# Kernel optimization log

Hardware: AMD Instinct MI355X
Metric: run time of the kernel (lower is better)

The kernel has to match this reference:

```python
import jax, jax.numpy as jnp
import numpy as np

DIM = 2048
ATT_DIM = 2048
N_HEADS = 16
HEAD_DIM = ATT_DIM // N_HEADS  # 128


def setup_inputs() -> dict:
    key = jax.random.key(0)
    k1, k2, k3 = jax.random.split(key, 3)
    tgt_len = 2048
    x = jax.random.normal(k1, (tgt_len, DIM), dtype=jnp.float32)
    # nn.Linear weights: [out_features, in_features], no bias
    w_in = jax.random.normal(k2, (3 * ATT_DIM, DIM), dtype=jnp.float32) * (1.0 / np.sqrt(DIM))
    w_out = jax.random.normal(k3, (DIM, ATT_DIM), dtype=jnp.float32) * (1.0 / np.sqrt(ATT_DIM))
    return {"x": x, "w_in": w_in, "w_out": w_out, "tgt_len": tgt_len}


def reference(x, w_in, w_out, tgt_len):
    # qkv projection: Linear -> x @ W^T, then split into thirds
    qkv = x @ w_in.T                      # [T, 3*att_dim]
    q, k, v = jnp.split(qkv, 3, axis=-1)  # each [T, att_dim]
    # [T, H, Dh] -> [H, T, Dh]
    q = q.reshape(tgt_len, N_HEADS, HEAD_DIM).transpose(1, 0, 2)
    k = k.reshape(tgt_len, N_HEADS, HEAD_DIM).transpose(1, 0, 2)
    v = v.reshape(tgt_len, N_HEADS, HEAD_DIM).transpose(1, 0, 2)
    scaling = 1.0 / jnp.sqrt(jnp.asarray(HEAD_DIM, dtype=x.dtype))
    scores = jnp.einsum("htd,hsd->hts", q, k) * scaling  # [H, T, T]
    attn = jax.nn.softmax(scores, axis=-1)
    ctx = jnp.einsum("hts,hsd->htd", attn, v)             # [H, T, Dh]
    ctx = ctx.transpose(1, 0, 2).reshape(tgt_len, ATT_DIM)
    return ctx @ w_out.T                                   # [T, dim]
```

## Files before the change

### kernel.cpp

```cpp
#include <hip/hip_runtime.h>

#define T_LEN 2048
#define DIM 2048
#define NH 16
#define HD 128
#define QKV_LD 6144

typedef __attribute__((ext_vector_type(8))) short short8;
typedef __attribute__((ext_vector_type(4))) float f32x4;
typedef __attribute__((ext_vector_type(4))) float float4v;
typedef __attribute__((ext_vector_type(4))) unsigned short ushort4v;
typedef __attribute__((ext_vector_type(2))) unsigned int uint2v;

static __device__ __forceinline__ unsigned short f2bf(float f) {
  unsigned u = __builtin_bit_cast(unsigned, f);
  u += 0x7fffu + ((u >> 16) & 1u);
  return (unsigned short)(u >> 16);
}

static __device__ __forceinline__ f32x4 mfma16(short8 a, short8 b, f32x4 c) {
  return __builtin_amdgcn_mfma_f32_16x16x32_bf16(a, b, c, 0, 0, 0);
}

#define GLDS16(SRC, DST)                                                            \
  __builtin_amdgcn_global_load_lds((__attribute__((address_space(1))) void*)(SRC),  \
                                   (__attribute__((address_space(3))) void*)(DST),  \
                                   16, 0, 0)

__global__ void cast_f32_bf16(const float* __restrict__ in,
                              unsigned short* __restrict__ out, int n4) {
  int i = blockIdx.x * blockDim.x + threadIdx.x;
  const int stride = gridDim.x * blockDim.x;
  for (; i < n4; i += stride) {
    float4v f = ((const float4v*)in)[i];
    ushort4v o;
    o.x = f2bf(f.x); o.y = f2bf(f.y); o.z = f2bf(f.z); o.w = f2bf(f.w);
    ((ushort4v*)out)[i] = o;
  }
}

template <int OUT_BF16>
__global__ __launch_bounds__(256) void gemm_bt_128(
    const unsigned short* __restrict__ A,
    const unsigned short* __restrict__ B,
    void* __restrict__ Cv, int M, int N, int K) {
  __shared__ unsigned short As[128 * 64];
  __shared__ unsigned short Bs[128 * 64];
  const int tid = threadIdx.x;
  const int wave = tid >> 6;
  const int lane = tid & 63;
  const int l15 = lane & 15, l16 = lane >> 4;
  const int bm = blockIdx.y * 128;
  const int bn = blockIdx.x * 128;
  const int wr = wave >> 1, wc = wave & 1;

  f32x4 acc[4][4] = {};

  int srow[4], scol[4];
#pragma unroll
  for (int i = 0; i < 4; ++i) {
    int lin = i * 4096 + tid * 16;
    int row = lin >> 7;
    int cb = lin & 127;
    srow[i] = row;
    scol[i] = (cb ^ ((row & 7) << 4)) >> 1;
  }

  for (int k0 = 0; k0 < K; k0 += 64) {
#pragma unroll
    for (int i = 0; i < 4; ++i) {
      GLDS16(A + (size_t)(bm + srow[i]) * K + k0 + scol[i], As + i * 2048 + wave * 512);
      GLDS16(B + (size_t)(bn + srow[i]) * K + k0 + scol[i], Bs + i * 2048 + wave * 512);
    }
    __syncthreads();
#pragma unroll
    for (int kk = 0; kk < 2; ++kk) {
      const int cb = kk * 64 + l16 * 16;
      short8 af[4], bfr[4];
#pragma unroll
      for (int m = 0; m < 4; ++m) {
        int row = wr * 64 + m * 16 + l15;
        af[m] = *(const short8*)((const char*)As + row * 128 + (cb ^ ((row & 7) << 4)));
      }
#pragma unroll
      for (int n = 0; n < 4; ++n) {
        int row = wc * 64 + n * 16 + l15;
        bfr[n] = *(const short8*)((const char*)Bs + row * 128 + (cb ^ ((row & 7) << 4)));
      }
#pragma unroll
      for (int m = 0; m < 4; ++m)
#pragma unroll
        for (int n = 0; n < 4; ++n)
          acc[m][n] = mfma16(af[m], bfr[n], acc[m][n]);
    }
    __syncthreads();
  }

#pragma unroll
  for (int m = 0; m < 4; ++m)
#pragma unroll
    for (int n = 0; n < 4; ++n) {
      int row = bm + wr * 64 + m * 16 + l16 * 4;
      int col = bn + wc * 64 + n * 16 + l15;
#pragma unroll
      for (int j = 0; j < 4; ++j) {
        if (OUT_BF16)
          ((unsigned short*)Cv)[(size_t)(row + j) * N + col] = f2bf(acc[m][n][j]);
        else
          ((float*)Cv)[(size_t)(row + j) * N + col] = acc[m][n][j];
      }
    }
}

__global__ __launch_bounds__(256) void transpose_v(
    const unsigned short* __restrict__ qkv, unsigned short* __restrict__ vt) {
  __shared__ unsigned short t[64 * 128];
  const int tid = threadIdx.x;
  const int h = blockIdx.y;
  const int s0 = blockIdx.x * 64;
#pragma unroll
  for (int i = 0; i < 4; ++i) {
    int lin = i * 2048 + tid * 8;
    int row = lin >> 7, col = lin & 127;
    char* dst = (char*)t + row * 256 + ((col * 2) ^ (((row >> 3) & 7) << 4));
    *(short8*)dst =
        *(const short8*)(qkv + (size_t)(s0 + row) * QKV_LD + 2 * DIM + h * HD + col);
  }
  __syncthreads();
#pragma unroll
  for (int i2 = 0; i2 < 4; ++i2) {
    int d = (tid >> 3) + i2 * 32;
    int sb = (tid & 7) * 8;
    short8 v;
#pragma unroll
    for (int j = 0; j < 8; ++j) {
      int s = sb + j;
      v[j] = *(const short*)((const char*)t + s * 256 + ((d * 2) ^ (((s >> 3) & 7) << 4)));
    }
    *(short8*)(vt + ((size_t)h * HD + d) * T_LEN + s0 + sb) = v;
  }
}

__global__ __launch_bounds__(256) void attn_fwd(
    const unsigned short* __restrict__ qkv,
    const unsigned short* __restrict__ vt,
    unsigned short* __restrict__ ctx) {
  __shared__ unsigned short Ks[2][64 * 128];
  __shared__ unsigned short Vs[2][128 * 64];
  __shared__ unsigned short Ps[4 * 16 * 64];
  const int tid = threadIdx.x;
  const int wave = tid >> 6;
  const int lane = tid & 63;
  const int l15 = lane & 15, l16 = lane >> 4;
  const int h = blockIdx.y;
  const int q0 = blockIdx.x * 64 + wave * 16;
  const float SCL = 0.08838834764831845f * 1.4426950408889634f;

  short8 qf[4];
#pragma unroll
  for (int kk = 0; kk < 4; ++kk)
    qf[kk] = *(const short8*)(qkv + (size_t)(q0 + l15) * QKV_LD + h * HD + kk * 32 + l16 * 8);

  f32x4 acc_o[8] = {};
  float m_r = -1e30f;
  float l_r = 0.f;

  int krow[4], kcol[4], vrow[4], vcol[4];
#pragma unroll
  for (int i = 0; i < 4; ++i) {
    int lin = i * 4096 + tid * 16;
    int r = lin >> 8;
    int cb = lin & 255;
    krow[i] = r; kcol[i] = (cb ^ ((r & 7) << 4)) >> 1;
    r = lin >> 7;
    cb = lin & 127;
    vrow[i] = r; vcol[i] = (cb ^ ((r & 7) << 4)) >> 1;
  }
  const unsigned short* kbase = qkv + 2048 + h * HD;
  const unsigned short* vbase = vt + (size_t)h * HD * T_LEN;

#define STAGE_KV(BUF, S0)                                                              \
  do {                                                                                 \
    _Pragma("unroll")                                                                  \
    for (int i = 0; i < 4; ++i) {                                                      \
      GLDS16(kbase + (size_t)((S0) + krow[i]) * QKV_LD + kcol[i],                      \
             Ks[BUF] + i * 2048 + wave * 512);                                         \
      GLDS16(vbase + (size_t)vrow[i] * T_LEN + (S0) + vcol[i],                         \
             Vs[BUF] + i * 2048 + wave * 512);                                         \
    }                                                                                  \
  } while (0)

  STAGE_KV(0, 0);
  __syncthreads();

  const int NT = T_LEN / 64;
  int cur = 0;
  for (int t = 0; t < NT; ++t) {
    if (t + 1 < NT) STAGE_KV(cur ^ 1, (t + 1) * 64);

    const unsigned short* ks = Ks[cur];
    const unsigned short* vs = Vs[cur];

    f32x4 st[4] = {};
#pragma unroll
    for (int c = 0; c < 4; ++c) {
#pragma unroll
      for (int kk = 0; kk < 4; ++kk) {
        int row = c * 16 + l15;
        int cb = kk * 64 + l16 * 16;
        short8 kf = *(const short8*)((const char*)ks + row * 256 + (cb ^ ((row & 7) << 4)));
        st[c] = mfma16(kf, qf[kk], st[c]);
      }
    }

    float pmax = -1e30f;
#pragma unroll
    for (int c = 0; c < 4; ++c)
#pragma unroll
      for (int j = 0; j < 4; ++j)
        pmax = fmaxf(pmax, st[c][j]);
    pmax *= SCL;
    pmax = fmaxf(pmax, __shfl_xor(pmax, 16));
    pmax = fmaxf(pmax, __shfl_xor(pmax, 32));

    if (!__all(pmax - m_r <= 8.0f)) {
      float nm = fmaxf(m_r, pmax);
      float corr = __builtin_amdgcn_exp2f(m_r - nm);
      m_r = nm;
      l_r *= corr;
      float cj[4];
#pragma unroll
      for (int j = 0; j < 4; ++j) cj[j] = __shfl(corr, l16 * 4 + j);
#pragma unroll
      for (int d = 0; d < 8; ++d)
#pragma unroll
        for (int j = 0; j < 4; ++j) acc_o[d][j] *= cj[j];
    }

    float p[4][4];
    float tsum = 0.f;
#pragma unroll
    for (int c = 0; c < 4; ++c)
#pragma unroll
      for (int j = 0; j < 4; ++j) {
        p[c][j] = __builtin_amdgcn_exp2f(st[c][j] * SCL - m_r);
        tsum += p[c][j];
      }
    tsum += __shfl_xor(tsum, 16);
    tsum += __shfl_xor(tsum, 32);
    l_r += tsum;

    char* pbase = (char*)Ps + wave * 2048;
#pragma unroll
    for (int c = 0; c < 4; ++c) {
      uint2v w;
      w.x = (unsigned)f2bf(p[c][0]) | ((unsigned)f2bf(p[c][1]) << 16);
      w.y = (unsigned)f2bf(p[c][2]) | ((unsigned)f2bf(p[c][3]) << 16);
      int off = l15 * 128 + c * 32 + l16 * 8;
      *(uint2v*)(pbase + (off ^ ((l15 & 7) << 4))) = w;
    }

#pragma unroll
    for (int kk = 0; kk < 2; ++kk) {
      int cb = kk * 64 + l16 * 16;
      short8 pa = *(const short8*)(pbase + l15 * 128 + (cb ^ ((l15 & 7) << 4)));
#pragma unroll
      for (int d = 0; d < 8; ++d) {
        int row = d * 16 + l15;
        short8 vb = *(const short8*)((const char*)vs + row * 128 + (cb ^ ((row & 7) << 4)));
        acc_o[d] = mfma16(pa, vb, acc_o[d]);
      }
    }

    __syncthreads();
    cur ^= 1;
  }
#undef STAGE_KV

  float lq[4];
#pragma unroll
  for (int j = 0; j < 4; ++j) lq[j] = 1.0f / __shfl(l_r, l16 * 4 + j);
#pragma unroll
  for (int d = 0; d < 8; ++d)
#pragma unroll
    for (int j = 0; j < 4; ++j) {
      int row = q0 + l16 * 4 + j;
      int col = h * HD + d * 16 + l15;
      ctx[(size_t)row * DIM + col] = f2bf(acc_o[d][j] * lq[j]);
    }
}

extern "C" void kernel_launch(void* const* d_in, const int* in_sizes, int n_in,
                              void* d_out, int out_size, void* d_ws, size_t ws_size,
                              hipStream_t stream) {
  const float* x = (const float*)d_in[0];
  const float* w_in = (const float*)d_in[1];
  const float* w_out = (const float*)d_in[2];

  char* ws = (char*)d_ws;
  unsigned short* xbf  = (unsigned short*)(ws + 0);
  unsigned short* wibf = (unsigned short*)(ws + 8388608);
  unsigned short* wobf = (unsigned short*)(ws + 33554432);
  unsigned short* qkv  = (unsigned short*)(ws + 41943040);
  unsigned short* ctx  = (unsigned short*)(ws + 67108864);
  unsigned short* vt   = (unsigned short*)(ws + 75497472);

  cast_f32_bf16<<<2048, 256, 0, stream>>>(x, xbf, (T_LEN * DIM) / 4);
  cast_f32_bf16<<<2048, 256, 0, stream>>>(w_in, wibf, (3 * DIM * DIM) / 4);
  cast_f32_bf16<<<2048, 256, 0, stream>>>(w_out, wobf, (DIM * DIM) / 4);

  gemm_bt_128<1><<<dim3(48, 16), 256, 0, stream>>>(xbf, wibf, (void*)qkv, T_LEN, 3 * DIM, DIM);
  transpose_v<<<dim3(32, 16), 256, 0, stream>>>(qkv, vt);
  attn_fwd<<<dim3(32, 16), 256, 0, stream>>>(qkv, vt, ctx);
  gemm_bt_128<0><<<dim3(16, 16), 256, 0, stream>>>(ctx, wobf, d_out, T_LEN, DIM, DIM);
}
```

Baseline: 189.8 us.

## Single-buffer K/V staging, swizzle workgroup order, and tree-reduce max and sum

Drops the K/V double buffer. Each iteration now loads its tile into a single LDS buffer, with a barrier before compute, using precomputed incremented pointers. This halves LDS use to raise occupancy, but loses the load/compute overlap within a block. It also remaps workgroup IDs so neighbouring blocks span different heads, and rewrites the row-max and row-sum reductions as shallower trees (max3, pairwise adds) to cut dependency chains.

```diff
diff --git a/kernel.cpp b/kernel.cpp
--- a/kernel.cpp
+++ b/kernel.cpp
@@ -16,6 +16,10 @@
   unsigned u = __builtin_bit_cast(unsigned, f);
   u += 0x7fffu + ((u >> 16) & 1u);
   return (unsigned short)(u >> 16);
+}
+
+static __device__ __forceinline__ float max3f(float a, float b, float c) {
+  return fmaxf(fmaxf(a, b), c);
 }
 
 static __device__ __forceinline__ f32x4 mfma16(short8 a, short8 b, f32x4 c) {
@@ -145,15 +149,18 @@
     const unsigned short* __restrict__ qkv,
     const unsigned short* __restrict__ vt,
     unsigned short* __restrict__ ctx) {
-  __shared__ unsigned short Ks[2][64 * 128];
-  __shared__ unsigned short Vs[2][128 * 64];
+  __shared__ unsigned short Ks[64 * 128];
+  __shared__ unsigned short Vs[128 * 64];
   __shared__ unsigned short Ps[4 * 16 * 64];
   const int tid = threadIdx.x;
   const int wave = tid >> 6;
   const int lane = tid & 63;
   const int l15 = lane & 15, l16 = lane >> 4;
-  const int h = blockIdx.y;
-  const int q0 = blockIdx.x * 64 + wave * 16;
+
+  const int wg = blockIdx.y * 32 + blockIdx.x;
+  const int swz = (wg & 7) * 64 + (wg >> 3);
+  const int h = swz >> 5;
+  const int q0 = (swz & 31) * 64 + wave * 16;
   const float SCL = 0.08838834764831845f * 1.4426950408889634f;
 
   short8 qf[4];
@@ -165,41 +172,29 @@
   float m_r = -1e30f;
   float l_r = 0.f;
 
-  int krow[4], kcol[4], vrow[4], vcol[4];
+  const unsigned short* kp[4];
+  const unsigned short* vp[4];
 #pragma unroll
   for (int i = 0; i < 4; ++i) {
     int lin = i * 4096 + tid * 16;
     int r = lin >> 8;
     int cb = lin & 255;
-    krow[i] = r; kcol[i] = (cb ^ ((r & 7) << 4)) >> 1;
+    kp[i] = qkv + 2048 + h * HD + (size_t)r * QKV_LD + ((cb ^ ((r & 7) << 4)) >> 1);
     r = lin >> 7;
     cb = lin & 127;
-    vrow[i] = r; vcol[i] = (cb ^ ((r & 7) << 4)) >> 1;
-  }
-  const unsigned short* kbase = qkv + 2048 + h * HD;
-  const unsigned short* vbase = vt + (size_t)h * HD * T_LEN;
-
-#define STAGE_KV(BUF, S0)                                                              \
-  do {                                                                                 \
-    _Pragma("unroll")                                                                  \
-    for (int i = 0; i < 4; ++i) {                                                      \
-      GLDS16(kbase + (size_t)((S0) + krow[i]) * QKV_LD + kcol[i],                      \
-             Ks[BUF] + i * 2048 + wave * 512);                                         \
-      GLDS16(vbase + (size_t)vrow[i] * T_LEN + (S0) + vcol[i],                         \
-             Vs[BUF] + i * 2048 + wave * 512);                                         \
-    }                                                                                  \
-  } while (0)
-
-  STAGE_KV(0, 0);
-  __syncthreads();
+    vp[i] = vt + (size_t)h * HD * T_LEN + (size_t)r * T_LEN + ((cb ^ ((r & 7) << 4)) >> 1);
+  }
 
   const int NT = T_LEN / 64;
-  int cur = 0;
   for (int t = 0; t < NT; ++t) {
-    if (t + 1 < NT) STAGE_KV(cur ^ 1, (t + 1) * 64);
-
-    const unsigned short* ks = Ks[cur];
-    const unsigned short* vs = Vs[cur];
+#pragma unroll
+    for (int i = 0; i < 4; ++i) {
+      GLDS16(kp[i], Ks + i * 2048 + wave * 512);
+      GLDS16(vp[i], Vs + i * 2048 + wave * 512);
+      kp[i] += 64 * QKV_LD;
+      vp[i] += 64;
+    }
+    __syncthreads();
 
     f32x4 st[4] = {};
 #pragma unroll
@@ -208,17 +203,17 @@
       for (int kk = 0; kk < 4; ++kk) {
         int row = c * 16 + l15;
         int cb = kk * 64 + l16 * 16;
-        short8 kf = *(const short8*)((const char*)ks + row * 256 + (cb ^ ((row & 7) << 4)));
+        short8 kf = *(const short8*)((const char*)Ks + row * 256 + (cb ^ ((row & 7) << 4)));
         st[c] = mfma16(kf, qf[kk], st[c]);
       }
     }
 
-    float pmax = -1e30f;
-#pragma unroll
-    for (int c = 0; c < 4; ++c)
-#pragma unroll
-      for (int j = 0; j < 4; ++j)
-        pmax = fmaxf(pmax, st[c][j]);
+    float ma = max3f(st[0][0], st[0][1], st[0][2]);
+    float mb = max3f(st[0][3], st[1][0], st[1][1]);
+    float mc = max3f(st[1][2], st[1][3], st[2][0]);
+    float md = max3f(st[2][1], st[2][2], st[2][3]);
+    float me = max3f(st[3][0], st[3][1], st[3][2]);
+    float pmax = fmaxf(max3f(ma, mb, mc), max3f(md, me, st[3][3]));
     pmax *= SCL;
     pmax = fmaxf(pmax, __shfl_xor(pmax, 16));
     pmax = fmaxf(pmax, __shfl_xor(pmax, 32));
@@ -238,14 +233,16 @@
     }
 
     float p[4][4];
-    float tsum = 0.f;
 #pragma unroll
     for (int c = 0; c < 4; ++c)
 #pragma unroll
-      for (int j = 0; j < 4; ++j) {
+      for (int j = 0; j < 4; ++j)
         p[c][j] = __builtin_amdgcn_exp2f(st[c][j] * SCL - m_r);
-        tsum += p[c][j];
-      }
+    float s01 = (p[0][0] + p[0][1]) + (p[0][2] + p[0][3]);
+    float s23 = (p[1][0] + p[1][1]) + (p[1][2] + p[1][3]);
+    float s45 = (p[2][0] + p[2][1]) + (p[2][2] + p[2][3]);
+    float s67 = (p[3][0] + p[3][1]) + (p[3][2] + p[3][3]);
+    float tsum = (s01 + s23) + (s45 + s67);
     tsum += __shfl_xor(tsum, 16);
     tsum += __shfl_xor(tsum, 32);
     l_r += tsum;
@@ -267,15 +264,13 @@
 #pragma unroll
       for (int d = 0; d < 8; ++d) {
         int row = d * 16 + l15;
-        short8 vb = *(const short8*)((const char*)vs + row * 128 + (cb ^ ((row & 7) << 4)));
+        short8 vb = *(const short8*)((const char*)Vs + row * 128 + (cb ^ ((row & 7) << 4)));
         acc_o[d] = mfma16(pa, vb, acc_o[d]);
       }
     }
 
     __syncthreads();
-    cur ^= 1;
-  }
-#undef STAGE_KV
+  }
 
   float lq[4];
 #pragma unroll
```

Result: slower. 194.6 us (+2.5%).

## Add 256x256 pipelined QKV GEMM and tune attention scheduling with XCD swizzle

Applied to the files above, without the earlier changes.

Replaces the 128x128 QKV projection GEMM with a new 256x256 tile, 512-thread kernel. It double-buffers A/B panels via direct global-to-LDS loads, interleaves loads with MFMA phases under explicit barriers and vmcnt waits, and remaps workgroups across XCDs. The attention kernel gains an XCD-aware block swizzle, raised wave priority around its MFMA sections, and tree-shaped max and sum reductions. The larger tile is meant to raise arithmetic intensity and L2 locality, at the cost of fewer workgroups (192) and a hand-tuned schedule that depends on exact outstanding-load counts.

```diff
diff --git a/kernel.cpp b/kernel.cpp
--- a/kernel.cpp
+++ b/kernel.cpp
@@ -16,6 +16,10 @@
   unsigned u = __builtin_bit_cast(unsigned, f);
   u += 0x7fffu + ((u >> 16) & 1u);
   return (unsigned short)(u >> 16);
+}
+
+static __device__ __forceinline__ float max3f(float a, float b, float c) {
+  return fmaxf(fmaxf(a, b), c);
 }
 
 static __device__ __forceinline__ f32x4 mfma16(short8 a, short8 b, f32x4 c) {
@@ -37,6 +41,171 @@
     o.x = f2bf(f.x); o.y = f2bf(f.y); o.z = f2bf(f.z); o.w = f2bf(f.w);
     ((ushort4v*)out)[i] = o;
   }
+}
+
+template <int OUT_BF16>
+__global__ __launch_bounds__(512) void gemm_bt_256(
+    const unsigned short* __restrict__ A,
+    const unsigned short* __restrict__ B,
+    void* __restrict__ Cv, int M, int N, int K) {
+  __shared__ unsigned short As[2][2][8192];
+  __shared__ unsigned short Bs[2][2][8192];
+  const int tid = threadIdx.x;
+  const int wave = tid >> 6;
+  const int lane = tid & 63;
+  const int l15 = lane & 15, l16 = lane >> 4;
+  const int wr = wave >> 2;
+  const int wc = wave & 3;
+
+  const int nby = M >> 8;
+  const int nwg = gridDim.x * gridDim.y;
+  const int wg = blockIdx.y * gridDim.x + blockIdx.x;
+  const int cpx = nwg >> 3;
+  const int swz = (wg & 7) * cpx + (wg >> 3);
+  const int bm = (swz % nby) * 256;
+  const int bn = (swz / nby) * 256;
+
+  const int arow0 = wave * 8 + (lane >> 3);
+  const int acol = (((lane & 7) * 16) ^ ((lane >> 3) << 4)) >> 1;
+  const unsigned short* apan = A + (size_t)bm * K;
+  const unsigned short* bpan = B + (size_t)bn * K;
+
+#define STG(ARR, SRCP, BUF, H, KOFF)                                           \
+  do {                                                                         \
+    GLDS16(SRCP + (size_t)((H)*128 + arow0) * K + (KOFF) + acol,               \
+           &ARR[BUF][H][wave * 512]);                                          \
+    GLDS16(SRCP + (size_t)((H)*128 + 64 + arow0) * K + (KOFF) + acol,          \
+           &ARR[BUF][H][4096 + wave * 512]);                                   \
+  } while (0)
+
+  f32x4 acc[8][4] = {};
+  const char* Ah;
+  const char* Bh;
+
+  const int NT = K / 64;
+  const int NI = NT / 2;
+
+  STG(Bs, bpan, 0, 0, 0); STG(Bs, bpan, 0, 1, 0);
+  STG(As, apan, 0, 0, 0); STG(As, apan, 0, 1, 0);
+  STG(Bs, bpan, 1, 0, 64); STG(Bs, bpan, 1, 1, 64);
+
+  short8 bf[4][2];
+  short8 af[2][2];
+
+#define READ_A(BASE, MM0)                                                       \
+  do {                                                                          \
+    _Pragma("unroll") for (int mm = 0; mm < 2; ++mm)                            \
+    _Pragma("unroll") for (int kk = 0; kk < 2; ++kk) {                          \
+      int row = ((MM0) + mm) * 16 + l15;                                        \
+      int cb = kk * 64 + l16 * 16;                                              \
+      af[mm][kk] = *(const short8*)((BASE) + row * 128 + (cb ^ ((row & 7) << 4))); \
+    }                                                                           \
+  } while (0)
+
+#define READ_B(BASE)                                                            \
+  do {                                                                          \
+    _Pragma("unroll") for (int n = 0; n < 4; ++n)                               \
+    _Pragma("unroll") for (int kk = 0; kk < 2; ++kk) {                          \
+      int row = (wc & 1) * 64 + n * 16 + l15;                                   \
+      int cb = kk * 64 + l16 * 16;                                              \
+      bf[n][kk] = *(const short8*)((BASE) + row * 128 + (cb ^ ((row & 7) << 4))); \
+    }                                                                           \
+  } while (0)
+
+#define MFMA16X(MM0)                                                            \
+  do {                                                                          \
+    __builtin_amdgcn_s_setprio(1);                                              \
+    _Pragma("unroll") for (int kk = 0; kk < 2; ++kk)                            \
+    _Pragma("unroll") for (int mm = 0; mm < 2; ++mm)                            \
+    _Pragma("unroll") for (int n = 0; n < 4; ++n)                               \
+      acc[(MM0) + mm][n] = mfma16(af[mm][kk], bf[n][kk], acc[(MM0) + mm][n]);   \
+    __builtin_amdgcn_s_setprio(0);                                              \
+  } while (0)
+
+#define BAR() __builtin_amdgcn_s_barrier()
+#define VMCNT6() asm volatile("s_waitcnt vmcnt(6)" ::: "memory")
+
+  for (int i = 0; i < NI; ++i) {
+    const int k0 = i * 128;
+    const int kA1 = k0 + 64;
+    const int kN0 = min(k0 + 128, K - 64);
+    const int kN1 = min(k0 + 192, K - 64);
+    const int b0 = 0, b1 = 1;
+
+    Ah = (const char*)As[b0][wr];
+    Bh = (const char*)Bs[b0][wc >> 1];
+
+    STG(As, apan, b1, 0, kA1);
+    VMCNT6();
+    BAR();
+    READ_B(Bh);
+    READ_A(Ah, 0);
+    MFMA16X(0);
+    BAR();
+    READ_A(Ah, 2);
+    STG(As, apan, b1, 1, kA1);
+    BAR();
+    MFMA16X(2);
+    BAR();
+    READ_A(Ah, 4);
+    STG(Bs, bpan, b0, 0, kN0);
+    BAR();
+    MFMA16X(4);
+    BAR();
+    READ_A(Ah, 6);
+    STG(Bs, bpan, b0, 1, kN0);
+    BAR();
+    MFMA16X(6);
+    BAR();
+
+    Ah = (const char*)As[b1][wr];
+    Bh = (const char*)Bs[b1][wc >> 1];
+
+    STG(As, apan, b0, 0, kN0);
+    VMCNT6();
+    BAR();
+    READ_B(Bh);
+    READ_A(Ah, 0);
+    MFMA16X(0);
+    BAR();
+    READ_A(Ah, 2);
+    STG(As, apan, b0, 1, kN0);
+    BAR();
+    MFMA16X(2);
+    BAR();
+    READ_A(Ah, 4);
+    STG(Bs, bpan, b1, 0, kN1);
+    BAR();
+    MFMA16X(4);
+    BAR();
+    READ_A(Ah, 6);
+    STG(Bs, bpan, b1, 1, kN1);
+    BAR();
+    MFMA16X(6);
+    BAR();
+  }
+  asm volatile("s_waitcnt vmcnt(0)" ::: "memory");
+
+#pragma unroll
+  for (int m = 0; m < 8; ++m)
+#pragma unroll
+    for (int n = 0; n < 4; ++n) {
+      int row = bm + wr * 128 + m * 16 + l16 * 4;
+      int col = bn + wc * 64 + n * 16 + l15;
+#pragma unroll
+      for (int j = 0; j < 4; ++j) {
+        if (OUT_BF16)
+          ((unsigned short*)Cv)[(size_t)(row + j) * N + col] = f2bf(acc[m][n][j]);
+        else
+          ((float*)Cv)[(size_t)(row + j) * N + col] = acc[m][n][j];
+      }
+    }
+#undef STG
+#undef READ_A
+#undef READ_B
+#undef MFMA16X
+#undef BAR
+#undef VMCNT6
 }
 
 template <int OUT_BF16>
@@ -152,8 +321,11 @@
   const int wave = tid >> 6;
   const int lane = tid & 63;
   const int l15 = lane & 15, l16 = lane >> 4;
-  const int h = blockIdx.y;
-  const int q0 = blockIdx.x * 64 + wave * 16;
+
+  const int wg = blockIdx.y * 32 + blockIdx.x;
+  const int swz = (wg & 7) * 64 + (wg >> 3);
+  const int h = swz >> 5;
+  const int q0 = (swz & 31) * 64 + wave * 16;
   const float SCL = 0.08838834764831845f * 1.4426950408889634f;
 
   short8 qf[4];
@@ -202,6 +374,7 @@
     const unsigned short* vs = Vs[cur];
 
     f32x4 st[4] = {};
+    __builtin_amdgcn_s_setprio(1);
 #pragma unroll
     for (int c = 0; c < 4; ++c) {
 #pragma unroll
@@ -212,14 +385,14 @@
         st[c] = mfma16(kf, qf[kk], st[c]);
       }
     }
-
-    float pmax = -1e30f;
-#pragma unroll
-    for (int c = 0; c < 4; ++c)
-#pragma unroll
-      for (int j = 0; j < 4; ++j)
-        pmax = fmaxf(pmax, st[c][j]);
-    pmax *= SCL;
+    __builtin_amdgcn_s_setprio(0);
+
+    float ma = max3f(st[0][0], st[0][1], st[0][2]);
+    float mb = max3f(st[0][3], st[1][0], st[1][1]);
+    float mc = max3f(st[1][2], st[1][3], st[2][0]);
+    float md = max3f(st[2][1], st[2][2], st[2][3]);
+    float me = max3f(st[3][0], st[3][1], st[3][2]);
+    float pmax = fmaxf(max3f(ma, mb, mc), max3f(md, me, st[3][3])) * SCL;
     pmax = fmaxf(pmax, __shfl_xor(pmax, 16));
     pmax = fmaxf(pmax, __shfl_xor(pmax, 32));
 
@@ -238,14 +411,16 @@
     }
 
     float p[4][4];
-    float tsum = 0.f;
 #pragma unroll
     for (int c = 0; c < 4; ++c)
 #pragma unroll
-      for (int j = 0; j < 4; ++j) {
+      for (int j = 0; j < 4; ++j)
         p[c][j] = __builtin_amdgcn_exp2f(st[c][j] * SCL - m_r);
-        tsum += p[c][j];
-      }
+    float s01 = (p[0][0] + p[0][1]) + (p[0][2] + p[0][3]);
+    float s23 = (p[1][0] + p[1][1]) + (p[1][2] + p[1][3]);
+    float s45 = (p[2][0] + p[2][1]) + (p[2][2] + p[2][3]);
+    float s67 = (p[3][0] + p[3][1]) + (p[3][2] + p[3][3]);
+    float tsum = (s01 + s23) + (s45 + s67);
     tsum += __shfl_xor(tsum, 16);
     tsum += __shfl_xor(tsum, 32);
     l_r += tsum;
@@ -260,6 +435,7 @@
       *(uint2v*)(pbase + (off ^ ((l15 & 7) << 4))) = w;
     }
 
+    __builtin_amdgcn_s_setprio(1);
 #pragma unroll
     for (int kk = 0; kk < 2; ++kk) {
       int cb = kk * 64 + l16 * 16;
@@ -271,6 +447,7 @@
         acc_o[d] = mfma16(pa, vb, acc_o[d]);
       }
     }
+    __builtin_amdgcn_s_setprio(0);
 
     __syncthreads();
     cur ^= 1;
@@ -309,7 +486,7 @@
   cast_f32_bf16<<<2048, 256, 0, stream>>>(w_in, wibf, (3 * DIM * DIM) / 4);
   cast_f32_bf16<<<2048, 256, 0, stream>>>(w_out, wobf, (DIM * DIM) / 4);
 
-  gemm_bt_128<1><<<dim3(48, 16), 256, 0, stream>>>(xbf, wibf, (void*)qkv, T_LEN, 3 * DIM, DIM);
+  gemm_bt_256<1><<<dim3(24, 8), 512, 0, stream>>>(xbf, wibf, (void*)qkv, T_LEN, 3 * DIM, DIM);
   transpose_v<<<dim3(32, 16), 256, 0, stream>>>(qkv, vt);
   attn_fwd<<<dim3(32, 16), 256, 0, stream>>>(qkv, vt, ctx);
   gemm_bt_128<0><<<dim3(16, 16), 256, 0, stream>>>(ctx, wobf, d_out, T_LEN, DIM, DIM);
```

Result: slower. 208.5 us (+9.9%).
